# Kernel tuning notes

Measured on AMD Instinct MI355X. Metric: run time of the kernel, lower is better.

Reference implementation:

```python
import jax, jax.numpy as jnp
import numpy as np


def log_g(x):
    # torch: where(x>=0, log(relu(x)+0.5), -softplus(-x))
    return jnp.where(x >= 0, jnp.log(jnp.maximum(x, 0.0) + 0.5), -jax.nn.softplus(-x))


def parallel_scan_log(log_coeffs, log_values):
    # log_coeffs: [B, T, H], log_values: [B, T+1, H]
    a_star = jnp.cumsum(log_coeffs, axis=1)
    a_star = jnp.pad(a_star, ((0, 0), (1, 0), (0, 0)))  # [B, T+1, H]
    log_h0_plus_b_star = jax.lax.cumlogsumexp(log_values - a_star, axis=1)
    return jnp.exp(a_star + log_h0_plus_b_star)


def setup_inputs() -> dict:
    key = jax.random.key(0)
    B, T, I, H = 8, 4096, 1024, 1024
    k1, k2, k3, k4, k5, k6 = jax.random.split(key, 6)
    scale = 1.0 / np.sqrt(I)
    return {
        "x": jax.random.normal(k1, (B, T, I), dtype=jnp.float32),
        "h_0": jax.random.normal(k2, (B, H), dtype=jnp.float32),
        "W_z": jax.random.uniform(k3, (H, I), jnp.float32, -scale, scale),
        "b_z": jax.random.uniform(k4, (H,), jnp.float32, -scale, scale),
        "W_h": jax.random.uniform(k5, (H, I), jnp.float32, -scale, scale),
        "b_h": jax.random.uniform(k6, (H,), jnp.float32, -scale, scale),
    }


def reference(x, h_0, W_z, b_z, W_h, b_h):
    T = x.shape[1]
    k = jnp.einsum("bti,hi->bth", x, W_z) + b_z          # linear_z(x)
    log_z = -jax.nn.softplus(-k)
    log_coeffs = -jax.nn.softplus(k)
    log_h_0 = log_g(h_0)[:, None, :]                      # [B, 1, H]
    log_tilde_h = log_g(jnp.einsum("bti,hi->bth", x, W_h) + b_h)
    log_values = jnp.concatenate([log_h_0, log_z + log_tilde_h], axis=1)
    h = parallel_scan_log(log_coeffs, log_values)         # [B, T+1, H]
    return h[:, -T:, :]
```

## Files before the change

kernel.cpp:

```cpp
#include <hip/hip_runtime.h>
#include <hip/hip_bf16.h>
#include <math.h>

typedef _Float16 half8_t __attribute__((ext_vector_type(8)));
typedef _Float16 half4_t __attribute__((ext_vector_type(4)));
typedef float    floatx4 __attribute__((ext_vector_type(4)));

#define GLOAD16(gp, lp) __builtin_amdgcn_global_load_lds( \
    (const __attribute__((address_space(1))) void*)(gp),  \
    (__attribute__((address_space(3))) void*)(lp), 16, 0, 0)

static constexpr int Bc  = 8;
static constexpr int Tc  = 4096;
static constexpr int Ic  = 1024;
static constexpr int Hc  = 1024;
static constexpr int Mc  = Bc * Tc;
static constexpr int NCc = 64;
static constexpr int Lc  = Tc / NCc;

__global__ void cvt_kernel(const float* __restrict__ in, _Float16* __restrict__ out, long n)
{
    long i = ((long)blockIdx.x * blockDim.x + threadIdx.x) * 4;
    long stride = (long)gridDim.x * blockDim.x * 4;
    for (; i < n; i += stride) {
        float4 v = *reinterpret_cast<const float4*>(in + i);
        half4_t h;
        h[0] = (_Float16)v.x; h[1] = (_Float16)v.y;
        h[2] = (_Float16)v.z; h[3] = (_Float16)v.w;
        *reinterpret_cast<half4_t*>(out + i) = h;
    }
}

__global__ __launch_bounds__(256) void dual_gemm_f16(
    const _Float16* __restrict__ A,
    const _Float16* __restrict__ Wz,
    const _Float16* __restrict__ Wh,
    const float* __restrict__ bz,
    const float* __restrict__ bh,
    float* __restrict__ Ck,
    float* __restrict__ Cp)
{
    constexpr int BM = 128, BN = 128, BK = 32, K = Ic, N = Hc;
    __shared__ __align__(16) _Float16 sA[BM * BK];
    __shared__ __align__(16) _Float16 sB[BN * BK];

    const _Float16* Bw  = blockIdx.z ? Wh : Wz;
    const float*   bias = blockIdx.z ? bh : bz;
    float*         C    = blockIdx.z ? Cp : Ck;

    const int tid  = threadIdx.x;
    const int lane = tid & 63;
    const int wave = tid >> 6;
    const int wr = wave >> 1, wc = wave & 1;
    const int m0 = blockIdx.y * BM, n0 = blockIdx.x * BN;

    const int srow = tid >> 2;
    const int schk = (tid & 3) * 8;
    const _Float16* gA = A  + (size_t)(m0 + srow) * K + schk;
    const _Float16* gB = Bw + (size_t)(n0 + srow) * K + schk;
    _Float16* lA = &sA[srow * BK + schk];
    _Float16* lB = &sB[srow * BK + schk];

    const int lrow = lane & 15;
    const int kch  = (lane >> 4) * 8;
    const half8_t* rA = (const half8_t*)&sA[(wr * 64 + lrow) * BK + kch];
    const half8_t* rB = (const half8_t*)&sB[(wc * 64 + lrow) * BK + kch];

    floatx4 zero4 = {0.f, 0.f, 0.f, 0.f};
    floatx4 acc[4][4];
#pragma unroll
    for (int m = 0; m < 4; m++)
#pragma unroll
        for (int n = 0; n < 4; n++) acc[m][n] = zero4;

    for (int kt = 0; kt < K; kt += BK) {
        GLOAD16(gA + kt,                  lA);
        GLOAD16(gA + kt + (size_t)64 * K, lA + 64 * BK);
        GLOAD16(gB + kt,                  lB);
        GLOAD16(gB + kt + (size_t)64 * K, lB + 64 * BK);
        __syncthreads();

        half8_t af[4], bf[4];
#pragma unroll
        for (int m = 0; m < 4; m++) af[m] = rA[m * 64];
#pragma unroll
        for (int n = 0; n < 4; n++) bf[n] = rB[n * 64];
#pragma unroll
        for (int m = 0; m < 4; m++)
#pragma unroll
            for (int n = 0; n < 4; n++)
                acc[m][n] = __builtin_amdgcn_mfma_f32_16x16x32_f16(af[m], bf[n], acc[m][n], 0, 0, 0);
        __syncthreads();
    }

    const int r0 = (lane >> 4) * 4;
#pragma unroll
    for (int n = 0; n < 4; n++) {
        const int col = n0 + wc * 64 + n * 16 + lrow;
        const float bv = bias[col];
#pragma unroll
        for (int m = 0; m < 4; m++) {
            const int row = m0 + wr * 64 + m * 16 + r0;
#pragma unroll
            for (int r = 0; r < 4; r++)
                C[(size_t)(row + r) * N + col] = acc[m][n][r] + bv;
        }
    }
}

__device__ __forceinline__ float sigm(float x) { return 1.0f / (1.0f + expf(-x)); }
__device__ __forceinline__ float g_fn(float x) { return x >= 0.0f ? x + 0.5f : sigm(x); }
__device__ __forceinline__ void fv_from_kp(float kk, float pp, float& f, float& v)
{
    float ek = expf(kk);
    f = 1.0f / (1.0f + ek);
    float z = 1.0f - f;
    v = z * g_fn(pp);
}

__global__ void scanA(const float* __restrict__ kb, const float* __restrict__ pb,
                      float* __restrict__ Fb, float* __restrict__ Sb)
{
    const int b = blockIdx.z, c = blockIdx.y;
    const int h = blockIdx.x * blockDim.x + threadIdx.x;
    size_t base = ((size_t)b * Tc + (size_t)c * Lc) * Hc + h;
    float F = 1.0f, S = 0.0f;
    for (int t = 0; t < Lc; t++) {
        float kk = kb[base + (size_t)t * Hc];
        float pp = pb[base + (size_t)t * Hc];
        float f, v; fv_from_kp(kk, pp, f, v);
        S = fmaf(f, S, v);
        F *= f;
    }
    size_t ci = ((size_t)b * NCc + c) * Hc + h;
    Fb[ci] = F; Sb[ci] = S;
}

__global__ void scanB(const float* __restrict__ h0, const float* __restrict__ Fb,
                      const float* __restrict__ Sb, float* __restrict__ Cin)
{
    const int idx = blockIdx.x * blockDim.x + threadIdx.x;
    const int b = idx >> 10, h = idx & 1023;
    float carry = g_fn(h0[(size_t)b * Hc + h]);
    for (int c = 0; c < NCc; c++) {
        size_t ci = ((size_t)b * NCc + c) * Hc + h;
        Cin[ci] = carry;
        carry = fmaf(Fb[ci], carry, Sb[ci]);
    }
}

__global__ void scanC(const float* __restrict__ kb, const float* __restrict__ pb,
                      const float* __restrict__ Cin, float* __restrict__ out)
{
    const int b = blockIdx.z, c = blockIdx.y;
    const int h = blockIdx.x * blockDim.x + threadIdx.x;
    size_t base = ((size_t)b * Tc + (size_t)c * Lc) * Hc + h;
    float hr = Cin[((size_t)b * NCc + c) * Hc + h];
    for (int t = 0; t < Lc; t++) {
        float kk = kb[base + (size_t)t * Hc];
        float pp = pb[base + (size_t)t * Hc];
        float f, v; fv_from_kp(kk, pp, f, v);
        hr = fmaf(f, hr, v);
        out[base + (size_t)t * Hc] = hr;
    }
}

extern "C" void kernel_launch(void* const* d_in, const int* in_sizes, int n_in,
                              void* d_out, int out_size, void* d_ws, size_t ws_size,
                              hipStream_t stream)
{
    const float* x  = (const float*)d_in[0];
    const float* h0 = (const float*)d_in[1];
    const float* Wz = (const float*)d_in[2];
    const float* bz = (const float*)d_in[3];
    const float* Wh = (const float*)d_in[4];
    const float* bh = (const float*)d_in[5];
    float* out = (float*)d_out;

    char* ws = (char*)d_ws;
    _Float16* x16  = (_Float16*)ws;
    _Float16* w16z = (_Float16*)(ws + 67108864);
    _Float16* w16h = w16z + (size_t)Hc * Ic;
    float* kbuf = (float*)(ws + 71303168);
    float* pbuf = (float*)(ws + 71303168 + 134217728);
    float* Fb   = (float*)(ws + 339738624ULL);
    float* Sb   = (float*)(ws + 341835776ULL);
    float* Cin  = (float*)(ws + 343932928ULL);

    cvt_kernel<<<2048, 256, 0, stream>>>(x,  x16,  (long)Mc * Ic);
    cvt_kernel<<<256,  256, 0, stream>>>(Wz, w16z, (long)Hc * Ic);
    cvt_kernel<<<256,  256, 0, stream>>>(Wh, w16h, (long)Hc * Ic);

    dim3 ggrid(Hc / 128, Mc / 128, 2);
    dual_gemm_f16<<<ggrid, 256, 0, stream>>>(x16, w16z, w16h, bz, bh, kbuf, pbuf);

    dim3 sgrid(Hc / 256, NCc, Bc);
    scanA<<<sgrid, 256, 0, stream>>>(kbuf, pbuf, Fb, Sb);
    scanB<<<32, 256, 0, stream>>>(h0, Fb, Sb, Cin);
    scanC<<<sgrid, 256, 0, stream>>>(kbuf, pbuf, Cin, out);
}
```

Before: 613.6 us.

## Fuse dual GEMM sharing A tile, double-buffer LDS, store fp16 intermediates, vectorize scans

The GEMM now computes both projections in one 512-thread block that shares the A tile in LDS, double-buffers the K loop and remaps block IDs for cache locality. The k and p intermediates are written as fp16 instead of fp32, which halves the traffic into and out of the scan kernels. The scan kernels process 8 channels per thread with vector loads and stores, use 128 chunks, and switch to fast __expf. In exchange, storing the pre-activations in fp16 and using the approximate exp lowers precision. Larger LDS use per block may also reduce occupancy.

Measured after the change: 504.1 us. -17.9%, faster.

```diff
diff --git a/kernel.cpp b/kernel.cpp
--- a/kernel.cpp
+++ b/kernel.cpp
@@ -15,8 +15,8 @@
 static constexpr int Ic  = 1024;
 static constexpr int Hc  = 1024;
 static constexpr int Mc  = Bc * Tc;
-static constexpr int NCc = 64;
-static constexpr int Lc  = Tc / NCc;
+static constexpr int NC2 = 128;
+static constexpr int L2c = Tc / NC2;
 
 __global__ void cvt_kernel(const float* __restrict__ in, _Float16* __restrict__ out, long n)
 {
@@ -31,55 +31,65 @@
     }
 }
 
-__global__ __launch_bounds__(256) void dual_gemm_f16(
+__global__ __launch_bounds__(512) void dual_gemm_f16(
     const _Float16* __restrict__ A,
     const _Float16* __restrict__ Wz,
     const _Float16* __restrict__ Wh,
     const float* __restrict__ bz,
     const float* __restrict__ bh,
-    float* __restrict__ Ck,
-    float* __restrict__ Cp)
-{
-    constexpr int BM = 128, BN = 128, BK = 32, K = Ic, N = Hc;
-    __shared__ __align__(16) _Float16 sA[BM * BK];
-    __shared__ __align__(16) _Float16 sB[BN * BK];
-
-    const _Float16* Bw  = blockIdx.z ? Wh : Wz;
-    const float*   bias = blockIdx.z ? bh : bz;
-    float*         C    = blockIdx.z ? Cp : Ck;
+    _Float16* __restrict__ k16,
+    _Float16* __restrict__ p16)
+{
+    constexpr int BK = 32, K = Ic, N = Hc, NSTEP = K / BK;
+    __shared__ __align__(16) _Float16 sA [2][128 * BK];
+    __shared__ __align__(16) _Float16 sBz[2][128 * BK];
+    __shared__ __align__(16) _Float16 sBh[2][128 * BK];
+
+    const int bid     = blockIdx.x;
+    const int logical = (bid & 7) * 256 + (bid >> 3);
+    const int n0 = (logical & 7) * 128;
+    const int m0 = (logical >> 3) * 128;
 
     const int tid  = threadIdx.x;
     const int lane = tid & 63;
     const int wave = tid >> 6;
-    const int wr = wave >> 1, wc = wave & 1;
-    const int m0 = blockIdx.y * BM, n0 = blockIdx.x * BN;
+    const int zsel = wave >> 2;
+    const int wr = (wave >> 1) & 1, wc = wave & 1;
 
     const int srow = tid >> 2;
     const int schk = (tid & 3) * 8;
-    const _Float16* gA = A  + (size_t)(m0 + srow) * K + schk;
-    const _Float16* gB = Bw + (size_t)(n0 + srow) * K + schk;
-    _Float16* lA = &sA[srow * BK + schk];
-    _Float16* lB = &sB[srow * BK + schk];
+    const int soff = srow * BK + schk;
+    const _Float16* gA  = A  + (size_t)(m0 + srow) * K + schk;
+    const _Float16* gBz = Wz + (size_t)(n0 + srow) * K + schk;
+    const _Float16* gBh = Wh + (size_t)(n0 + srow) * K + schk;
 
     const int lrow = lane & 15;
     const int kch  = (lane >> 4) * 8;
-    const half8_t* rA = (const half8_t*)&sA[(wr * 64 + lrow) * BK + kch];
-    const half8_t* rB = (const half8_t*)&sB[(wc * 64 + lrow) * BK + kch];
-
-    floatx4 zero4 = {0.f, 0.f, 0.f, 0.f};
+    const _Float16* sBsel = zsel ? &sBh[0][0] : &sBz[0][0];
+    const int aoff = (wr * 64 + lrow) * BK + kch;
+    const int boff = (wc * 64 + lrow) * BK + kch;
+
     floatx4 acc[4][4];
 #pragma unroll
     for (int m = 0; m < 4; m++)
 #pragma unroll
-        for (int n = 0; n < 4; n++) acc[m][n] = zero4;
-
-    for (int kt = 0; kt < K; kt += BK) {
-        GLOAD16(gA + kt,                  lA);
-        GLOAD16(gA + kt + (size_t)64 * K, lA + 64 * BK);
-        GLOAD16(gB + kt,                  lB);
-        GLOAD16(gB + kt + (size_t)64 * K, lB + 64 * BK);
-        __syncthreads();
-
+        for (int n = 0; n < 4; n++) acc[m][n] = (floatx4){0.f, 0.f, 0.f, 0.f};
+
+    GLOAD16(gA,  &sA [0][soff]);
+    GLOAD16(gBz, &sBz[0][soff]);
+    GLOAD16(gBh, &sBh[0][soff]);
+    __syncthreads();
+
+    int buf = 0;
+    for (int ki = 0; ki < NSTEP; ki++) {
+        if (ki + 1 < NSTEP) {
+            const int kt = (ki + 1) * BK;
+            GLOAD16(gA  + kt, &sA [buf ^ 1][soff]);
+            GLOAD16(gBz + kt, &sBz[buf ^ 1][soff]);
+            GLOAD16(gBh + kt, &sBh[buf ^ 1][soff]);
+        }
+        const half8_t* rA = (const half8_t*)&sA[buf][aoff];
+        const half8_t* rB = (const half8_t*)(sBsel + (size_t)buf * (128 * BK) + boff);
         half8_t af[4], bf[4];
 #pragma unroll
         for (int m = 0; m < 4; m++) af[m] = rA[m * 64];
@@ -91,8 +101,11 @@
             for (int n = 0; n < 4; n++)
                 acc[m][n] = __builtin_amdgcn_mfma_f32_16x16x32_f16(af[m], bf[n], acc[m][n], 0, 0, 0);
         __syncthreads();
-    }
-
+        buf ^= 1;
+    }
+
+    _Float16* C = zsel ? p16 : k16;
+    const float* bias = zsel ? bh : bz;
     const int r0 = (lane >> 4) * 4;
 #pragma unroll
     for (int n = 0; n < 4; n++) {
@@ -103,65 +116,83 @@
             const int row = m0 + wr * 64 + m * 16 + r0;
 #pragma unroll
             for (int r = 0; r < 4; r++)
-                C[(size_t)(row + r) * N + col] = acc[m][n][r] + bv;
-        }
-    }
-}
-
-__device__ __forceinline__ float sigm(float x) { return 1.0f / (1.0f + expf(-x)); }
+                C[(size_t)(row + r) * N + col] = (_Float16)(acc[m][n][r] + bv);
+        }
+    }
+}
+
+__device__ __forceinline__ float sigm(float x) { return 1.0f / (1.0f + __expf(-x)); }
 __device__ __forceinline__ float g_fn(float x) { return x >= 0.0f ? x + 0.5f : sigm(x); }
 __device__ __forceinline__ void fv_from_kp(float kk, float pp, float& f, float& v)
 {
-    float ek = expf(kk);
+    float ek = __expf(kk);
     f = 1.0f / (1.0f + ek);
     float z = 1.0f - f;
     v = z * g_fn(pp);
 }
 
-__global__ void scanA(const float* __restrict__ kb, const float* __restrict__ pb,
-                      float* __restrict__ Fb, float* __restrict__ Sb)
-{
-    const int b = blockIdx.z, c = blockIdx.y;
-    const int h = blockIdx.x * blockDim.x + threadIdx.x;
-    size_t base = ((size_t)b * Tc + (size_t)c * Lc) * Hc + h;
-    float F = 1.0f, S = 0.0f;
-    for (int t = 0; t < Lc; t++) {
-        float kk = kb[base + (size_t)t * Hc];
-        float pp = pb[base + (size_t)t * Hc];
-        float f, v; fv_from_kp(kk, pp, f, v);
-        S = fmaf(f, S, v);
-        F *= f;
-    }
-    size_t ci = ((size_t)b * NCc + c) * Hc + h;
-    Fb[ci] = F; Sb[ci] = S;
-}
-
-__global__ void scanB(const float* __restrict__ h0, const float* __restrict__ Fb,
+__global__ __launch_bounds__(128) void scanA(const _Float16* __restrict__ k16,
+                                             const _Float16* __restrict__ p16,
+                                             float* __restrict__ Fb, float* __restrict__ Sb)
+{
+    const int b = blockIdx.y, c = blockIdx.x;
+    const int h0 = threadIdx.x * 8;
+    size_t base = ((size_t)b * Tc + (size_t)c * L2c) * Hc + h0;
+    float F[8], S[8];
+#pragma unroll
+    for (int j = 0; j < 8; j++) { F[j] = 1.0f; S[j] = 0.0f; }
+    for (int t = 0; t < L2c; t++) {
+        half8_t k8 = *reinterpret_cast<const half8_t*>(k16 + base + (size_t)t * Hc);
+        half8_t p8 = *reinterpret_cast<const half8_t*>(p16 + base + (size_t)t * Hc);
+#pragma unroll
+        for (int j = 0; j < 8; j++) {
+            float f, v; fv_from_kp((float)k8[j], (float)p8[j], f, v);
+            S[j] = fmaf(f, S[j], v);
+            F[j] *= f;
+        }
+    }
+    size_t ci = ((size_t)b * NC2 + c) * Hc + h0;
+#pragma unroll
+    for (int j = 0; j < 8; j++) { Fb[ci + j] = F[j]; Sb[ci + j] = S[j]; }
+}
+
+__global__ void scanB(const float* __restrict__ h0p, const float* __restrict__ Fb,
                       const float* __restrict__ Sb, float* __restrict__ Cin)
 {
     const int idx = blockIdx.x * blockDim.x + threadIdx.x;
     const int b = idx >> 10, h = idx & 1023;
-    float carry = g_fn(h0[(size_t)b * Hc + h]);
-    for (int c = 0; c < NCc; c++) {
-        size_t ci = ((size_t)b * NCc + c) * Hc + h;
+    float carry = g_fn(h0p[(size_t)b * Hc + h]);
+    for (int c = 0; c < NC2; c++) {
+        size_t ci = ((size_t)b * NC2 + c) * Hc + h;
         Cin[ci] = carry;
         carry = fmaf(Fb[ci], carry, Sb[ci]);
     }
 }
 
-__global__ void scanC(const float* __restrict__ kb, const float* __restrict__ pb,
-                      const float* __restrict__ Cin, float* __restrict__ out)
-{
-    const int b = blockIdx.z, c = blockIdx.y;
-    const int h = blockIdx.x * blockDim.x + threadIdx.x;
-    size_t base = ((size_t)b * Tc + (size_t)c * Lc) * Hc + h;
-    float hr = Cin[((size_t)b * NCc + c) * Hc + h];
-    for (int t = 0; t < Lc; t++) {
-        float kk = kb[base + (size_t)t * Hc];
-        float pp = pb[base + (size_t)t * Hc];
-        float f, v; fv_from_kp(kk, pp, f, v);
-        hr = fmaf(f, hr, v);
-        out[base + (size_t)t * Hc] = hr;
+__global__ __launch_bounds__(128) void scanC(const _Float16* __restrict__ k16,
+                                             const _Float16* __restrict__ p16,
+                                             const float* __restrict__ Cin,
+                                             float* __restrict__ out)
+{
+    const int b = blockIdx.y, c = blockIdx.x;
+    const int h0 = threadIdx.x * 8;
+    size_t base = ((size_t)b * Tc + (size_t)c * L2c) * Hc + h0;
+    size_t ci = ((size_t)b * NC2 + c) * Hc + h0;
+    float hr[8];
+#pragma unroll
+    for (int j = 0; j < 8; j++) hr[j] = Cin[ci + j];
+    for (int t = 0; t < L2c; t++) {
+        half8_t k8 = *reinterpret_cast<const half8_t*>(k16 + base + (size_t)t * Hc);
+        half8_t p8 = *reinterpret_cast<const half8_t*>(p16 + base + (size_t)t * Hc);
+#pragma unroll
+        for (int j = 0; j < 8; j++) {
+            float f, v; fv_from_kp((float)k8[j], (float)p8[j], f, v);
+            hr[j] = fmaf(f, hr[j], v);
+        }
+        float4 o0 = make_float4(hr[0], hr[1], hr[2], hr[3]);
+        float4 o1 = make_float4(hr[4], hr[5], hr[6], hr[7]);
+        *reinterpret_cast<float4*>(out + base + (size_t)t * Hc)     = o0;
+        *reinterpret_cast<float4*>(out + base + (size_t)t * Hc + 4) = o1;
     }
 }
 
@@ -179,23 +210,22 @@
 
     char* ws = (char*)d_ws;
     _Float16* x16  = (_Float16*)ws;
-    _Float16* w16z = (_Float16*)(ws + 67108864);
-    _Float16* w16h = w16z + (size_t)Hc * Ic;
-    float* kbuf = (float*)(ws + 71303168);
-    float* pbuf = (float*)(ws + 71303168 + 134217728);
-    float* Fb   = (float*)(ws + 339738624ULL);
-    float* Sb   = (float*)(ws + 341835776ULL);
-    float* Cin  = (float*)(ws + 343932928ULL);
+    _Float16* w16z = (_Float16*)(ws + 67108864ULL);
+    _Float16* w16h = (_Float16*)(ws + 69206016ULL);
+    _Float16* k16  = (_Float16*)(ws + 71303168ULL);
+    _Float16* p16  = (_Float16*)(ws + 138412032ULL);
+    float* Fb  = (float*)(ws + 205520896ULL);
+    float* Sb  = (float*)(ws + 209715200ULL);
+    float* Cin = (float*)(ws + 213909504ULL);
 
     cvt_kernel<<<2048, 256, 0, stream>>>(x,  x16,  (long)Mc * Ic);
     cvt_kernel<<<256,  256, 0, stream>>>(Wz, w16z, (long)Hc * Ic);
     cvt_kernel<<<256,  256, 0, stream>>>(Wh, w16h, (long)Hc * Ic);
 
-    dim3 ggrid(Hc / 128, Mc / 128, 2);
-    dual_gemm_f16<<<ggrid, 256, 0, stream>>>(x16, w16z, w16h, bz, bh, kbuf, pbuf);
-
-    dim3 sgrid(Hc / 256, NCc, Bc);
-    scanA<<<sgrid, 256, 0, stream>>>(kbuf, pbuf, Fb, Sb);
+    dual_gemm_f16<<<2048, 512, 0, stream>>>(x16, w16z, w16h, bz, bh, k16, p16);
+
+    dim3 sgrid(NC2, Bc);
+    scanA<<<sgrid, 128, 0, stream>>>(k16, p16, Fb, Sb);
     scanB<<<32, 256, 0, stream>>>(h0, Fb, Sb, Cin);
-    scanC<<<sgrid, 256, 0, stream>>>(kbuf, pbuf, Cin, out);
-}
+    scanC<<<sgrid, 128, 0, stream>>>(k16, p16, Cin, out);
+}
```
